# Kernel optimization log

Measured on AMD Instinct MI355X. Metric: run time of the kernel, lower is better.

The kernel has to match this reference:

```python
import jax, jax.numpy as jnp
import numpy as np
import math

STAGE_NUM = 5


def _l2norm(t, axis):
    return t / (1e-6 + jnp.linalg.norm(t, axis=axis, keepdims=True))


def setup_inputs() -> dict:
    key = jax.random.key(0)
    ks = jax.random.split(key, 6)
    b, n, c, h, w, k = 8, 5, 512, 32, 32, 64
    x = jax.random.normal(ks[0], (b, n, c, h, w), dtype=jnp.float32)
    mu = jax.random.normal(ks[1], (1, c, k), dtype=jnp.float32) * math.sqrt(2.0 / k)
    mu = _l2norm(mu, axis=1)
    # 1x1 convs init: normal(0, sqrt(2/(1*1*out_channels)))
    std = math.sqrt(2.0 / c)
    conv1_w = jax.random.normal(ks[2], (c, c), dtype=jnp.float32) * std  # [out,in]
    conv1_b = jnp.zeros((c,), dtype=jnp.float32)
    conv2_w = jax.random.normal(ks[3], (c, c), dtype=jnp.float32) * std
    bn_gamma = jnp.ones((c,), dtype=jnp.float32)
    bn_beta = jnp.zeros((c,), dtype=jnp.float32)
    return {"x": x, "mu": mu, "conv1_w": conv1_w, "conv1_b": conv1_b,
            "conv2_w": conv2_w, "bn_gamma": bn_gamma, "bn_beta": bn_beta}


def reference(x, mu, conv1_w, conv1_b, conv2_w, bn_gamma, bn_beta):
    b, n, c, h, w = x.shape
    xf = x.reshape(b * n, c, h, w)
    idn = xf
    # conv1: 1x1 conv with bias
    y = jnp.einsum('bchw,dc->bdhw', xf, conv1_w) + conv1_b[None, :, None, None]
    # [b, c, N] with N = n*h*w
    y = y.reshape(b, n, c, h, w).transpose(0, 2, 1, 3, 4).reshape(b, c, n * h * w)
    mu_b = jnp.broadcast_to(mu, (b, c, mu.shape[2]))
    z = None
    # EM iterations (no_grad in original; fwd-only so just compute)
    for _ in range(STAGE_NUM):
        z = jax.nn.softmax(jnp.einsum('bcn,bck->bnk', y, mu_b), axis=2)  # [b,N,k]
        z_ = z / (1e-6 + z.sum(axis=1, keepdims=True))
        mu_b = _l2norm(jnp.einsum('bcn,bnk->bck', y, z_), axis=1)
    # reconstruction: mu @ z^T -> [b,c,N]
    rec = jnp.einsum('bck,bnk->bcn', mu_b, z)
    rec = jax.nn.relu(rec.reshape(b, c, n, h, w))
    rec = rec.transpose(0, 2, 1, 3, 4).reshape(b * n, c, h, w)
    # conv2 (no bias) + BatchNorm (training-mode batch stats)
    y2 = jnp.einsum('bchw,dc->bdhw', rec, conv2_w)
    mean = y2.mean(axis=(0, 2, 3), keepdims=True)
    var = y2.var(axis=(0, 2, 3), keepdims=True)
    y2 = (y2 - mean) * jax.lax.rsqrt(var + 1e-5)
    y2 = y2 * bn_gamma[None, :, None, None] + bn_beta[None, :, None, None]
    out = jax.nn.relu(y2 + idn).reshape(b, n, c, h, w)
    return out, mu_b
```

## Files before the change

### kernel.cpp

```cpp
#include <hip/hip_runtime.h>
#include <math.h>

#define CH 512
#define K 64
#define BB 8
#define NIMG 5
#define HW 1024
#define NP 5120
#define BI 40

typedef __attribute__((ext_vector_type(8))) _Float16 f16x8;
typedef __attribute__((ext_vector_type(4))) _Float16 f16x4;
typedef __attribute__((ext_vector_type(4))) float f32x4;
typedef __attribute__((ext_vector_type(8))) short s16x8;

#define AS1 __attribute__((address_space(1)))
#define AS3 __attribute__((address_space(3)))

__global__ __launch_bounds__(256) void wconv(const float* __restrict__ w,
                                             _Float16* __restrict__ o)
{
    int i = blockIdx.x * 256 + threadIdx.x;
    o[i] = (_Float16)w[i];
}

__global__ __launch_bounds__(256) void transpose_f16(
    const float* __restrict__ in, _Float16* __restrict__ out, int P)
{
    __shared__ float tile[64][65];
    int t = threadIdx.x;
    int p0 = blockIdx.x * 64, c0 = blockIdx.y * 64;
    long ibase = (long)blockIdx.z * CH * P;
    long obase = (long)blockIdx.z * P * CH;
    int pl = t & 63, chh = t >> 6;
    #pragma unroll
    for (int i = 0; i < 16; ++i)
        tile[chh + i * 4][pl] = in[ibase + (long)(c0 + chh + i * 4) * P + p0 + pl];
    __syncthreads();
    int cc = t & 31, pr = t >> 5;
    #pragma unroll
    for (int i = 0; i < 8; ++i) {
        int p = pr + i * 8;
        _Float16 lo = (_Float16)tile[cc * 2][p];
        _Float16 hi = (_Float16)tile[cc * 2 + 1][p];
        unsigned lob = (unsigned)*(unsigned short*)&lo;
        unsigned hib = (unsigned)*(unsigned short*)&hi;
        *(unsigned*)&out[obase + (long)(p0 + p) * CH + c0 + cc * 2] = lob | (hib << 16);
    }
}

__global__ __launch_bounds__(256) void bcast_mu2(const float* __restrict__ mu_in,
                                                 float* __restrict__ mu_cur,
                                                 _Float16* __restrict__ muT)
{
    int i = blockIdx.x * 256 + threadIdx.x;
    float v = mu_in[i & 32767];
    mu_cur[i] = v;
    int b = i >> 15, ck = i & 32767, c = ck >> 6, k = ck & 63;
    muT[((long)b << 15) + k * CH + c] = (_Float16)v;
}

__global__ __launch_bounds__(256) void conv_tile(
    const _Float16* __restrict__ Wh, const _Float16* __restrict__ inT,
    const float* __restrict__ bias, float* __restrict__ y2,
    _Float16* __restrict__ y16, _Float16* __restrict__ yT16, int mode)
{
    __shared__ _Float16 Wt[128 * 64];
    __shared__ _Float16 Xt[128 * 64];
    int t = threadIdx.x;
    int lane = t & 63, w = t >> 6;
    int l15 = lane & 15, l4 = lane >> 4;
    int wd = w & 1, wp = w >> 1;
    int bi = blockIdx.z;
    int d0 = blockIdx.y * 128;
    int pl0 = blockIdx.x * 128;
    long prow0 = (long)bi * HW + pl0;
    int ci_row = lane >> 3;
    int colb_phys = (lane & 7) * 16;

    f32x4 acc[4][4];
    #pragma unroll
    for (int ai = 0; ai < 4; ++ai)
        #pragma unroll
        for (int bj = 0; bj < 4; ++bj) acc[ai][bj] = (f32x4){0.f, 0.f, 0.f, 0.f};

    for (int c0 = 0; c0 < CH; c0 += 64) {
        __syncthreads();
        #pragma unroll
        for (int i = 0; i < 4; ++i) {
            int row = w * 32 + i * 8 + ci_row;
            int cb = colb_phys ^ ((row & 7) << 4);
            const _Float16* srcW = Wh + (long)(d0 + row) * CH + c0 + (cb >> 1);
            const _Float16* srcX = inT + (prow0 + row) * (long)CH + c0 + (cb >> 1);
            __builtin_amdgcn_global_load_lds((const AS1 void*)srcW,
                (AS3 void*)&Wt[(w * 32 + i * 8) * 64], 16, 0, 0);
            __builtin_amdgcn_global_load_lds((const AS1 void*)srcX,
                (AS3 void*)&Xt[(w * 32 + i * 8) * 64], 16, 0, 0);
        }
        __syncthreads();
        #pragma unroll
        for (int kk = 0; kk < 2; ++kk) {
            f16x8 af[4], bf[4];
            #pragma unroll
            for (int ai = 0; ai < 4; ++ai) {
                int row = wd * 64 + ai * 16 + l15;
                int cb = (kk * 64 + l4 * 16) ^ ((row & 7) << 4);
                af[ai] = *(const f16x8*)((const char*)Wt + row * 128 + cb);
            }
            #pragma unroll
            for (int bj = 0; bj < 4; ++bj) {
                int row = wp * 64 + bj * 16 + l15;
                int cb = (kk * 64 + l4 * 16) ^ ((row & 7) << 4);
                bf[bj] = *(const f16x8*)((const char*)Xt + row * 128 + cb);
            }
            #pragma unroll
            for (int ai = 0; ai < 4; ++ai)
                #pragma unroll
                for (int bj = 0; bj < 4; ++bj)
                    acc[ai][bj] = __builtin_amdgcn_mfma_f32_16x16x32_f16(
                        af[ai], bf[bj], acc[ai][bj], 0, 0, 0);
        }
    }

    int b = bi / NIMG, n = bi % NIMG;
    if (mode == 0) {
        #pragma unroll
        for (int ai = 0; ai < 4; ++ai) {
            int dd = d0 + wd * 64 + ai * 16 + l4 * 4;
            float b0 = bias[dd], b1 = bias[dd + 1], b2 = bias[dd + 2], b3 = bias[dd + 3];
            #pragma unroll
            for (int bj = 0; bj < 4; ++bj) {
                int pb = n * HW + pl0 + wp * 64 + bj * 16 + l15;
                f16x4 pk = { (_Float16)(acc[ai][bj][0] + b0), (_Float16)(acc[ai][bj][1] + b1),
                             (_Float16)(acc[ai][bj][2] + b2), (_Float16)(acc[ai][bj][3] + b3) };
                *(f16x4*)&yT16[((long)b * NP + pb) * CH + dd] = pk;
                long yb = ((long)b * CH + dd) * NP + pb;
                y16[yb] = pk[0];
                y16[yb + NP] = pk[1];
                y16[yb + 2 * NP] = pk[2];
                y16[yb + 3 * NP] = pk[3];
            }
        }
    } else {
        long obase = (long)bi * CH * HW;
        #pragma unroll
        for (int ai = 0; ai < 4; ++ai) {
            int dd = d0 + wd * 64 + ai * 16 + l4 * 4;
            #pragma unroll
            for (int bj = 0; bj < 4; ++bj) {
                int p = pl0 + wp * 64 + bj * 16 + l15;
                long o = obase + (long)dd * HW + p;
                y2[o] = acc[ai][bj][0];
                y2[o + HW] = acc[ai][bj][1];
                y2[o + 2 * HW] = acc[ai][bj][2];
                y2[o + 3 * HW] = acc[ai][bj][3];
            }
        }
    }
}

__global__ __launch_bounds__(256) void stage_z_mfma(
    const _Float16* __restrict__ yT, const _Float16* __restrict__ muT,
    _Float16* __restrict__ zT, _Float16* __restrict__ z16,
    float* __restrict__ zsum, int writeZ)
{
    __shared__ _Float16 ms[32768];
    int t = threadIdx.x;
    int w = t >> 6, lane = t & 63, l15 = lane & 15, l4 = lane >> 4;
    int p0 = blockIdx.x * 64;
    int b = blockIdx.y;
    const _Float16* mb = muT + ((long)b << 15);
    #pragma unroll
    for (int it = 0; it < 16; ++it) {
        int sl = t + it * 256;
        int cc = sl >> 8, j = (sl >> 6) & 3, ln = sl & 63;
        int rl15 = ln & 15, rl4 = ln >> 4;
        *(s16x8*)&ms[sl * 8] = *(const s16x8*)&mb[(rl15 + 16 * j) * CH + cc * 32 + rl4 * 8];
    }
    const _Float16* arow = yT + ((long)b * NP + p0 + w * 16 + l15) * CH + l4 * 8;
    f32x4 acc[4];
    #pragma unroll
    for (int j = 0; j < 4; ++j) acc[j] = (f32x4){0.f, 0.f, 0.f, 0.f};
    __syncthreads();
    #pragma unroll
    for (int cc = 0; cc < 16; ++cc) {
        f16x8 a = *(const f16x8*)(arow + cc * 32);
        #pragma unroll
        for (int j = 0; j < 4; ++j) {
            f16x8 bj = *(const f16x8*)&ms[((cc * 4 + j) * 64 + lane) * 8];
            acc[j] = __builtin_amdgcn_mfma_f32_16x16x32_f16(a, bj, acc[j], 0, 0, 0);
        }
    }
    float zv[4][4];
    #pragma unroll
    for (int i = 0; i < 4; ++i) {
        float m = fmaxf(fmaxf(acc[0][i], acc[1][i]), fmaxf(acc[2][i], acc[3][i]));
        #pragma unroll
        for (int off = 1; off < 16; off <<= 1) m = fmaxf(m, __shfl_xor(m, off, 64));
        float e0 = __expf(acc[0][i] - m);
        float e1 = __expf(acc[1][i] - m);
        float e2 = __expf(acc[2][i] - m);
        float e3 = __expf(acc[3][i] - m);
        float s = e0 + e1 + e2 + e3;
        #pragma unroll
        for (int off = 1; off < 16; off <<= 1) s += __shfl_xor(s, off, 64);
        float inv = 1.f / s;
        zv[0][i] = e0 * inv; zv[1][i] = e1 * inv; zv[2][i] = e2 * inv; zv[3][i] = e3 * inv;
    }
    int prow = p0 + w * 16 + l4 * 4;
    long ztbase = (long)b * K * NP;
    #pragma unroll
    for (int j = 0; j < 4; ++j) {
        f16x4 pk = { (_Float16)zv[j][0], (_Float16)zv[j][1],
                     (_Float16)zv[j][2], (_Float16)zv[j][3] };
        *(f16x4*)&zT[ztbase + (long)(l15 + 16 * j) * NP + prow] = pk;
    }
    if (writeZ) {
        long zbase = (long)b * NP * K;
        #pragma unroll
        for (int j = 0; j < 4; ++j)
            #pragma unroll
            for (int i = 0; i < 4; ++i)
                z16[zbase + (long)(prow + i) * K + l15 + 16 * j] = (_Float16)zv[j][i];
    }
    float part[4];
    #pragma unroll
    for (int j = 0; j < 4; ++j) {
        part[j] = zv[j][0] + zv[j][1] + zv[j][2] + zv[j][3];
        part[j] += __shfl_xor(part[j], 16, 64);
        part[j] += __shfl_xor(part[j], 32, 64);
    }
    __syncthreads();
    float* zred = (float*)ms;
    if (l4 == 0) {
        #pragma unroll
        for (int j = 0; j < 4; ++j) zred[w * 64 + l15 + 16 * j] = part[j];
    }
    __syncthreads();
    if (t < 64)
        atomicAdd(&zsum[b * 64 + t], zred[t] + zred[64 + t] + zred[128 + t] + zred[192 + t]);
}

__global__ __launch_bounds__(256) void stage_mu_mfma(
    const _Float16* __restrict__ y16, const _Float16* __restrict__ zT,
    float* __restrict__ macc)
{
    __shared__ _Float16 zs[2048];
    int t = threadIdx.x;
    int w = t >> 6, lane = t & 63, l15 = lane & 15, l4 = lane >> 4;
    int pc = blockIdx.x, ct = blockIdx.y, b = blockIdx.z;
    int pbase = pc * 640;
    const _Float16* zsrc = zT + (long)b * K * NP + (long)(l15 + 16 * w) * NP + l4 * 8;
    const _Float16* arow = y16 + ((long)b * CH + ct * 64 + w * 16 + l15) * NP + l4 * 8;
    f32x4 acc[4];
    #pragma unroll
    for (int j = 0; j < 4; ++j) acc[j] = (f32x4){0.f, 0.f, 0.f, 0.f};
    for (int p0 = pbase; p0 < pbase + 640; p0 += 32) {
        __syncthreads();
        *(s16x8*)&zs[t * 8] = *(const s16x8*)(zsrc + p0);
        __syncthreads();
        f16x8 a = *(const f16x8*)(arow + p0);
        #pragma unroll
        for (int j = 0; j < 4; ++j) {
            f16x8 bj = *(const f16x8*)&zs[(j * 64 + lane) * 8];
            acc[j] = __builtin_amdgcn_mfma_f32_16x16x32_f16(a, bj, acc[j], 0, 0, 0);
        }
    }
    float* mp = macc + ((long)pc * BB + b) * K * CH;
    #pragma unroll
    for (int j = 0; j < 4; ++j)
        *(f32x4*)&mp[(long)(l15 + 16 * j) * CH + ct * 64 + w * 16 + l4 * 4] = acc[j];
}

__global__ __launch_bounds__(256) void mu_norm2(
    const float* __restrict__ macc, const float* __restrict__ zsum,
    float* __restrict__ mu_cur, _Float16* __restrict__ mu16,
    _Float16* __restrict__ muT)
{
    int gw = blockIdx.x * 4 + (threadIdx.x >> 6);
    int lane = threadIdx.x & 63;
    int b = gw >> 6, k = gw & 63;
    float v[8];
    float s = 0.f;
    #pragma unroll
    for (int ci = 0; ci < 8; ++ci) {
        int c = ci * 64 + lane;
        float a = 0.f;
        #pragma unroll
        for (int pcc = 0; pcc < 8; ++pcc)
            a += macc[(((long)pcc * BB + b) * K + k) * CH + c];
        v[ci] = a; s += a * a;
    }
    #pragma unroll
    for (int off = 1; off < 64; off <<= 1) s += __shfl_xor(s, off, 64);
    float d = 1e-6f + zsum[b * 64 + k];
    float scale = 1.f / (1e-6f * d + sqrtf(s));
    long mb = (long)b << 15;
    #pragma unroll
    for (int ci = 0; ci < 8; ++ci) {
        int c = ci * 64 + lane;
        float m = v[ci] * scale;
        mu_cur[mb + (long)c * K + k] = m;
        mu16[mb + (long)c * K + k] = (_Float16)m;
        muT[mb + (long)k * CH + c] = (_Float16)m;
    }
}

__global__ __launch_bounds__(256) void rec_mfma(
    const _Float16* __restrict__ z16, const _Float16* __restrict__ mu16,
    _Float16* __restrict__ recT)
{
    __shared__ _Float16 rt[64 * 80];
    int t = threadIdx.x;
    int w = t >> 6, lane = t & 63, l15 = lane & 15, l4 = lane >> 4;
    int p0 = blockIdx.x * 64, ct = blockIdx.y, b = blockIdx.z;
    const _Float16* zb = z16 + (long)b * NP * K;
    const _Float16* mb = mu16 + ((long)b << 15) + (long)(ct * 64 + w * 16 + l15) * K + l4 * 8;
    f32x4 acc[4];
    #pragma unroll
    for (int pj = 0; pj < 4; ++pj) acc[pj] = (f32x4){0.f, 0.f, 0.f, 0.f};
    #pragma unroll
    for (int kc = 0; kc < 64; kc += 32) {
        f16x8 bfr = *(const f16x8*)(mb + kc);
        #pragma unroll
        for (int pj = 0; pj < 4; ++pj) {
            f16x8 a = *(const f16x8*)(zb + (long)(p0 + pj * 16 + l15) * K + kc + l4 * 8);
            acc[pj] = __builtin_amdgcn_mfma_f32_16x16x32_f16(a, bfr, acc[pj], 0, 0, 0);
        }
    }
    #pragma unroll
    for (int pj = 0; pj < 4; ++pj)
        #pragma unroll
        for (int i = 0; i < 4; ++i)
            rt[(pj * 16 + l4 * 4 + i) * 80 + w * 16 + l15] = (_Float16)fmaxf(acc[pj][i], 0.f);
    __syncthreads();
    #pragma unroll
    for (int it = 0; it < 2; ++it) {
        int l = t + it * 256;
        int row = l >> 3, s8 = l & 7;
        *(s16x8*)&recT[((long)b * NP + p0 + row) * CH + ct * 64 + s8 * 8] =
            *(const s16x8*)&rt[row * 80 + s8 * 8];
    }
}

__global__ __launch_bounds__(256) void bn_stats(const float* __restrict__ y2,
                                                float* __restrict__ stats,
                                                float* __restrict__ statsq)
{
    int d = blockIdx.x;
    int t = threadIdx.x;
    float s = 0.f, sq = 0.f;
    for (int idx = t; idx < BI * HW; idx += 256) {
        int bi = idx >> 10, hw = idx & 1023;
        float v = y2[(long)bi * CH * HW + (long)d * HW + hw];
        s += v; sq += v * v;
    }
    for (int off = 32; off; off >>= 1) {
        s += __shfl_xor(s, off, 64);
        sq += __shfl_xor(sq, off, 64);
    }
    __shared__ float ps[8];
    int wv = t >> 6, ln = t & 63;
    if (ln == 0) { ps[wv] = s; ps[4 + wv] = sq; }
    __syncthreads();
    if (t == 0) {
        stats[d]  = ps[0] + ps[1] + ps[2] + ps[3];
        statsq[d] = ps[4] + ps[5] + ps[6] + ps[7];
    }
}

__global__ __launch_bounds__(256) void final_kernel(
    const float* __restrict__ y2, const float* __restrict__ x,
    const float* __restrict__ stats, const float* __restrict__ statsq,
    const float* __restrict__ gamma, const float* __restrict__ beta,
    const float* __restrict__ mu_cur, float* __restrict__ out)
{
    long i = (long)blockIdx.x * 256 + threadIdx.x;
    const long NMAIN = (long)BI * CH * HW;
    if (i < NMAIN) {
        int d = (int)((i >> 10) & (CH - 1));
        float s = stats[d], sq = statsq[d];
        const float inv = 1.f / (float)(BI * HW);
        float mean = s * inv;
        float var = sq * inv - mean * mean;
        float rs = rsqrtf(var + 1e-5f);
        float v = (y2[i] - mean) * rs * gamma[d] + beta[d] + x[i];
        out[i] = fmaxf(v, 0.f);
    } else if (i < NMAIN + (long)BB * CH * K) {
        out[i] = mu_cur[i - NMAIN];
    }
}

extern "C" void kernel_launch(void* const* d_in, const int* in_sizes, int n_in,
                              void* d_out, int out_size, void* d_ws, size_t ws_size,
                              hipStream_t stream) {
    const float* x   = (const float*)d_in[0];
    const float* mu0 = (const float*)d_in[1];
    const float* w1  = (const float*)d_in[2];
    const float* b1  = (const float*)d_in[3];
    const float* w2  = (const float*)d_in[4];
    const float* gm  = (const float*)d_in[5];
    const float* bt  = (const float*)d_in[6];
    float* out = (float*)d_out;

    float* ws = (float*)d_ws;
    _Float16* y16h  = (_Float16*)(ws);
    _Float16* yT16h = (_Float16*)(ws + 10485760);
    _Float16* xTh   = (_Float16*)(ws + 20971520);
    _Float16* zTh   = (_Float16*)(ws + 20971520);
    _Float16* z16h  = (_Float16*)(ws + 22282240);
    float*    macc  = ws + 23592960;
    float*    mu_cur = ws + 31457280;
    _Float16* Wh1   = (_Float16*)(ws + 31719424);
    _Float16* Wh2   = (_Float16*)(ws + 31850496);
    _Float16* mu16h = (_Float16*)(ws + 31981568);
    _Float16* muTh  = (_Float16*)(ws + 32112640);
    float*    zsum  = ws + 32243712;
    float*    stats = ws + 32244224;
    float*    statsq = ws + 32244736;
    float* y2 = out;

    wconv<<<1024, 256, 0, stream>>>(w1, Wh1);
    wconv<<<1024, 256, 0, stream>>>(w2, Wh2);
    transpose_f16<<<dim3(16, 8, 40), 256, 0, stream>>>(x, xTh, HW);
    conv_tile<<<dim3(8, 4, 40), 256, 0, stream>>>(Wh1, xTh, b1, nullptr, y16h, yT16h, 0);
    bcast_mu2<<<1024, 256, 0, stream>>>(mu0, mu_cur, muTh);

    for (int s = 0; s < 5; ++s) {
        hipMemsetAsync(zsum, 0, 512 * sizeof(float), stream);
        stage_z_mfma<<<dim3(80, 8), 256, 0, stream>>>(yT16h, muTh, zTh, z16h, zsum, s == 4);
        stage_mu_mfma<<<dim3(8, 8, 8), 256, 0, stream>>>(y16h, zTh, macc);
        mu_norm2<<<128, 256, 0, stream>>>(macc, zsum, mu_cur, mu16h, muTh);
    }

    rec_mfma<<<dim3(80, 8, 8), 256, 0, stream>>>(z16h, mu16h, yT16h);
    conv_tile<<<dim3(8, 4, 40), 256, 0, stream>>>(Wh2, yT16h, nullptr, y2, nullptr, nullptr, 1);
    bn_stats<<<512, 256, 0, stream>>>(y2, stats, statsq);
    long total = (long)BI * CH * HW + (long)BB * CH * K;
    final_kernel<<<(int)((total + 255) / 256), 256, 0, stream>>>(
        y2, x, stats, statsq, gm, bt, mu_cur, out);
}
```

Baseline: 492.9 us.

## Double-buffer conv tiles, fuse BN stats into conv2, vectorize final pass

conv_tile now double-buffers its LDS tiles so the next channel slice loads while MFMAs run on the current one. In the conv2 mode it reduces per-channel sum and sum-of-squares in registers and accumulates them with atomics, which removes the separate bn_stats pass that re-read the whole fp32 output. stage_mu_mfma now processes 64 points per sync instead of 32, and final_kernel works on float4 vectors with a folded scale and bias. The per-stage zsum memsets are replaced by one upfront memset covering slices for all stages plus the stats buffers. The trade-off is more LDS per block and atomic contention on the stats arrays.

```diff
diff --git a/kernel.cpp b/kernel.cpp
--- a/kernel.cpp
+++ b/kernel.cpp
@@ -63,10 +63,11 @@
 __global__ __launch_bounds__(256) void conv_tile(
     const _Float16* __restrict__ Wh, const _Float16* __restrict__ inT,
     const float* __restrict__ bias, float* __restrict__ y2,
-    _Float16* __restrict__ y16, _Float16* __restrict__ yT16, int mode)
-{
-    __shared__ _Float16 Wt[128 * 64];
-    __shared__ _Float16 Xt[128 * 64];
+    _Float16* __restrict__ y16, _Float16* __restrict__ yT16,
+    float* __restrict__ stats, float* __restrict__ statsq, int mode)
+{
+    __shared__ _Float16 Wt[2][128 * 64];
+    __shared__ _Float16 Xt[2][128 * 64];
     int t = threadIdx.x;
     int lane = t & 63, w = t >> 6;
     int l15 = lane & 15, l4 = lane >> 4;
@@ -84,20 +85,26 @@
         #pragma unroll
         for (int bj = 0; bj < 4; ++bj) acc[ai][bj] = (f32x4){0.f, 0.f, 0.f, 0.f};
 
+#define STAGE(buf, cc0)                                                          \
+    {                                                                            \
+        _Pragma("unroll")                                                        \
+        for (int i = 0; i < 4; ++i) {                                            \
+            int row = w * 32 + i * 8 + ci_row;                                   \
+            int cb = colb_phys ^ ((row & 7) << 4);                               \
+            const _Float16* srcW = Wh + (long)(d0 + row) * CH + (cc0) + (cb >> 1);\
+            const _Float16* srcX = inT + (prow0 + row) * (long)CH + (cc0) + (cb >> 1);\
+            __builtin_amdgcn_global_load_lds((const AS1 void*)srcW,              \
+                (AS3 void*)&Wt[buf][(w * 32 + i * 8) * 64], 16, 0, 0);           \
+            __builtin_amdgcn_global_load_lds((const AS1 void*)srcX,              \
+                (AS3 void*)&Xt[buf][(w * 32 + i * 8) * 64], 16, 0, 0);           \
+        }                                                                        \
+    }
+
+    STAGE(0, 0)
+    __syncthreads();
     for (int c0 = 0; c0 < CH; c0 += 64) {
-        __syncthreads();
-        #pragma unroll
-        for (int i = 0; i < 4; ++i) {
-            int row = w * 32 + i * 8 + ci_row;
-            int cb = colb_phys ^ ((row & 7) << 4);
-            const _Float16* srcW = Wh + (long)(d0 + row) * CH + c0 + (cb >> 1);
-            const _Float16* srcX = inT + (prow0 + row) * (long)CH + c0 + (cb >> 1);
-            __builtin_amdgcn_global_load_lds((const AS1 void*)srcW,
-                (AS3 void*)&Wt[(w * 32 + i * 8) * 64], 16, 0, 0);
-            __builtin_amdgcn_global_load_lds((const AS1 void*)srcX,
-                (AS3 void*)&Xt[(w * 32 + i * 8) * 64], 16, 0, 0);
-        }
-        __syncthreads();
+        int cur = (c0 >> 6) & 1;
+        if (c0 + 64 < CH) STAGE(cur ^ 1, c0 + 64)
         #pragma unroll
         for (int kk = 0; kk < 2; ++kk) {
             f16x8 af[4], bf[4];
@@ -105,13 +112,13 @@
             for (int ai = 0; ai < 4; ++ai) {
                 int row = wd * 64 + ai * 16 + l15;
                 int cb = (kk * 64 + l4 * 16) ^ ((row & 7) << 4);
-                af[ai] = *(const f16x8*)((const char*)Wt + row * 128 + cb);
+                af[ai] = *(const f16x8*)((const char*)&Wt[cur][0] + row * 128 + cb);
             }
             #pragma unroll
             for (int bj = 0; bj < 4; ++bj) {
                 int row = wp * 64 + bj * 16 + l15;
                 int cb = (kk * 64 + l4 * 16) ^ ((row & 7) << 4);
-                bf[bj] = *(const f16x8*)((const char*)Xt + row * 128 + cb);
+                bf[bj] = *(const f16x8*)((const char*)&Xt[cur][0] + row * 128 + cb);
             }
             #pragma unroll
             for (int ai = 0; ai < 4; ++ai)
@@ -120,7 +127,9 @@
                     acc[ai][bj] = __builtin_amdgcn_mfma_f32_16x16x32_f16(
                         af[ai], bf[bj], acc[ai][bj], 0, 0, 0);
         }
-    }
+        __syncthreads();
+    }
+#undef STAGE
 
     int b = bi / NIMG, n = bi % NIMG;
     if (mode == 0) {
@@ -156,6 +165,25 @@
                 y2[o + 3 * HW] = acc[ai][bj][3];
             }
         }
+        #pragma unroll
+        for (int ai = 0; ai < 4; ++ai) {
+            #pragma unroll
+            for (int i = 0; i < 4; ++i) {
+                float s = acc[ai][0][i] + acc[ai][1][i] + acc[ai][2][i] + acc[ai][3][i];
+                float q = acc[ai][0][i] * acc[ai][0][i] + acc[ai][1][i] * acc[ai][1][i]
+                        + acc[ai][2][i] * acc[ai][2][i] + acc[ai][3][i] * acc[ai][3][i];
+                #pragma unroll
+                for (int off = 1; off < 16; off <<= 1) {
+                    s += __shfl_xor(s, off, 64);
+                    q += __shfl_xor(q, off, 64);
+                }
+                if (l15 == 0) {
+                    int dd = d0 + wd * 64 + ai * 16 + l4 * 4 + i;
+                    atomicAdd(&stats[dd], s);
+                    atomicAdd(&statsq[dd], q);
+                }
+            }
+        }
     }
 }
 
@@ -245,7 +273,7 @@
     const _Float16* __restrict__ y16, const _Float16* __restrict__ zT,
     float* __restrict__ macc)
 {
-    __shared__ _Float16 zs[2048];
+    __shared__ _Float16 zs[4096];
     int t = threadIdx.x;
     int w = t >> 6, lane = t & 63, l15 = lane & 15, l4 = lane >> 4;
     int pc = blockIdx.x, ct = blockIdx.y, b = blockIdx.z;
@@ -255,15 +283,19 @@
     f32x4 acc[4];
     #pragma unroll
     for (int j = 0; j < 4; ++j) acc[j] = (f32x4){0.f, 0.f, 0.f, 0.f};
-    for (int p0 = pbase; p0 < pbase + 640; p0 += 32) {
+    for (int p0 = pbase; p0 < pbase + 640; p0 += 64) {
         __syncthreads();
         *(s16x8*)&zs[t * 8] = *(const s16x8*)(zsrc + p0);
+        *(s16x8*)&zs[2048 + t * 8] = *(const s16x8*)(zsrc + p0 + 32);
         __syncthreads();
-        f16x8 a = *(const f16x8*)(arow + p0);
+        f16x8 a0 = *(const f16x8*)(arow + p0);
+        f16x8 a1 = *(const f16x8*)(arow + p0 + 32);
         #pragma unroll
         for (int j = 0; j < 4; ++j) {
-            f16x8 bj = *(const f16x8*)&zs[(j * 64 + lane) * 8];
-            acc[j] = __builtin_amdgcn_mfma_f32_16x16x32_f16(a, bj, acc[j], 0, 0, 0);
+            f16x8 bj0 = *(const f16x8*)&zs[(j * 64 + lane) * 8];
+            acc[j] = __builtin_amdgcn_mfma_f32_16x16x32_f16(a0, bj0, acc[j], 0, 0, 0);
+            f16x8 bj1 = *(const f16x8*)&zs[2048 + (j * 64 + lane) * 8];
+            acc[j] = __builtin_amdgcn_mfma_f32_16x16x32_f16(a1, bj1, acc[j], 0, 0, 0);
         }
     }
     float* mp = macc + ((long)pc * BB + b) * K * CH;
@@ -343,51 +375,35 @@
     }
 }
 
-__global__ __launch_bounds__(256) void bn_stats(const float* __restrict__ y2,
-                                                float* __restrict__ stats,
-                                                float* __restrict__ statsq)
-{
-    int d = blockIdx.x;
-    int t = threadIdx.x;
-    float s = 0.f, sq = 0.f;
-    for (int idx = t; idx < BI * HW; idx += 256) {
-        int bi = idx >> 10, hw = idx & 1023;
-        float v = y2[(long)bi * CH * HW + (long)d * HW + hw];
-        s += v; sq += v * v;
-    }
-    for (int off = 32; off; off >>= 1) {
-        s += __shfl_xor(s, off, 64);
-        sq += __shfl_xor(sq, off, 64);
-    }
-    __shared__ float ps[8];
-    int wv = t >> 6, ln = t & 63;
-    if (ln == 0) { ps[wv] = s; ps[4 + wv] = sq; }
-    __syncthreads();
-    if (t == 0) {
-        stats[d]  = ps[0] + ps[1] + ps[2] + ps[3];
-        statsq[d] = ps[4] + ps[5] + ps[6] + ps[7];
-    }
-}
-
 __global__ __launch_bounds__(256) void final_kernel(
     const float* __restrict__ y2, const float* __restrict__ x,
     const float* __restrict__ stats, const float* __restrict__ statsq,
     const float* __restrict__ gamma, const float* __restrict__ beta,
     const float* __restrict__ mu_cur, float* __restrict__ out)
 {
-    long i = (long)blockIdx.x * 256 + threadIdx.x;
-    const long NMAIN = (long)BI * CH * HW;
-    if (i < NMAIN) {
+    long i4 = (long)blockIdx.x * 256 + threadIdx.x;
+    const long NMAIN4 = (long)BI * CH * HW / 4;
+    if (i4 < NMAIN4) {
+        long i = i4 * 4;
         int d = (int)((i >> 10) & (CH - 1));
         float s = stats[d], sq = statsq[d];
         const float inv = 1.f / (float)(BI * HW);
         float mean = s * inv;
         float var = sq * inv - mean * mean;
         float rs = rsqrtf(var + 1e-5f);
-        float v = (y2[i] - mean) * rs * gamma[d] + beta[d] + x[i];
-        out[i] = fmaxf(v, 0.f);
-    } else if (i < NMAIN + (long)BB * CH * K) {
-        out[i] = mu_cur[i - NMAIN];
+        float g = rs * gamma[d];
+        float bb = beta[d] - mean * g;
+        float4 yv = *(const float4*)&y2[i];
+        float4 xv = *(const float4*)&x[i];
+        float4 ov;
+        ov.x = fmaxf(yv.x * g + bb + xv.x, 0.f);
+        ov.y = fmaxf(yv.y * g + bb + xv.y, 0.f);
+        ov.z = fmaxf(yv.z * g + bb + xv.z, 0.f);
+        ov.w = fmaxf(yv.w * g + bb + xv.w, 0.f);
+        *(float4*)&out[i] = ov;
+    } else {
+        long j = (i4 - NMAIN4) * 4;
+        *(float4*)&out[(long)BI * CH * HW + j] = *(const float4*)&mu_cur[j];
     }
 }
 
@@ -416,27 +432,30 @@
     _Float16* mu16h = (_Float16*)(ws + 31981568);
     _Float16* muTh  = (_Float16*)(ws + 32112640);
     float*    zsum  = ws + 32243712;
-    float*    stats = ws + 32244224;
-    float*    statsq = ws + 32244736;
+    float*    stats = ws + 32246272;
+    float*    statsq = ws + 32246784;
     float* y2 = out;
+
+    hipMemsetAsync(zsum, 0, 3584 * sizeof(float), stream);
 
     wconv<<<1024, 256, 0, stream>>>(w1, Wh1);
     wconv<<<1024, 256, 0, stream>>>(w2, Wh2);
     transpose_f16<<<dim3(16, 8, 40), 256, 0, stream>>>(x, xTh, HW);
-    conv_tile<<<dim3(8, 4, 40), 256, 0, stream>>>(Wh1, xTh, b1, nullptr, y16h, yT16h, 0);
+    conv_tile<<<dim3(8, 4, 40), 256, 0, stream>>>(Wh1, xTh, b1, nullptr, y16h, yT16h,
+                                                  nullptr, nullptr, 0);
     bcast_mu2<<<1024, 256, 0, stream>>>(mu0, mu_cur, muTh);
 
     for (int s = 0; s < 5; ++s) {
-        hipMemsetAsync(zsum, 0, 512 * sizeof(float), stream);
-        stage_z_mfma<<<dim3(80, 8), 256, 0, stream>>>(yT16h, muTh, zTh, z16h, zsum, s == 4);
+        stage_z_mfma<<<dim3(80, 8), 256, 0, stream>>>(yT16h, muTh, zTh, z16h,
+                                                      zsum + s * 512, s == 4);
         stage_mu_mfma<<<dim3(8, 8, 8), 256, 0, stream>>>(y16h, zTh, macc);
-        mu_norm2<<<128, 256, 0, stream>>>(macc, zsum, mu_cur, mu16h, muTh);
+        mu_norm2<<<128, 256, 0, stream>>>(macc, zsum + s * 512, mu_cur, mu16h, muTh);
     }
 
     rec_mfma<<<dim3(80, 8, 8), 256, 0, stream>>>(z16h, mu16h, yT16h);
-    conv_tile<<<dim3(8, 4, 40), 256, 0, stream>>>(Wh2, yT16h, nullptr, y2, nullptr, nullptr, 1);
-    bn_stats<<<512, 256, 0, stream>>>(y2, stats, statsq);
-    long total = (long)BI * CH * HW + (long)BB * CH * K;
-    final_kernel<<<(int)((total + 255) / 256), 256, 0, stream>>>(
+    conv_tile<<<dim3(8, 4, 40), 256, 0, stream>>>(Wh2, yT16h, nullptr, y2, nullptr, nullptr,
+                                                  stats, statsq, 1);
+    long total4 = ((long)BI * CH * HW + (long)BB * CH * K) / 4;
+    final_kernel<<<(int)((total4 + 255) / 256), 256, 0, stream>>>(
         y2, x, stats, statsq, gm, bt, mu_cur, out);
 }
```

Measured after the change: 464.7 us. 5.7% less time.
